# Optimization experiments

Hardware: AMD Instinct MI355X
Metric: run time of the kernel (lower is better)

Reference implementation:

```python
import jax, jax.numpy as jnp
import numpy as np

B, T, D = 4, 2048, 1024
EPS = 1e-5


def _layernorm(x, g, b):
    mu = jnp.mean(x, axis=-1, keepdims=True)
    var = jnp.var(x, axis=-1, keepdims=True)
    return (x - mu) * jax.lax.rsqrt(var + EPS) * g + b


def setup_inputs() -> dict:
    key = jax.random.key(0)
    ks = jax.random.split(key, 16)
    s = lambda fan_in: 1.0 / np.sqrt(fan_in)
    return {
        "x": jax.random.normal(ks[0], (B, T, D), dtype=jnp.float32),
        "ln1_g": jnp.ones((D,), jnp.float32),
        "ln1_b": jnp.zeros((D,), jnp.float32),
        "Wqkv": jax.random.uniform(ks[1], (D, 3 * D), jnp.float32, -s(D), s(D)),
        "bqkv": jnp.zeros((3 * D,), jnp.float32),
        "Wproj": jax.random.uniform(ks[2], (D, D), jnp.float32, -s(D), s(D)),
        "bproj": jnp.zeros((D,), jnp.float32),
        "ln2_g": jnp.ones((D,), jnp.float32),
        "ln2_b": jnp.zeros((D,), jnp.float32),
        "W1": jax.random.uniform(ks[3], (D, 4 * D), jnp.float32, -s(D), s(D)),
        "b1": jnp.zeros((4 * D,), jnp.float32),
        "W2": jax.random.uniform(ks[4], (4 * D, D), jnp.float32, -s(4 * D), s(4 * D)),
        "b2": jnp.zeros((D,), jnp.float32),
    }


def reference(x, ln1_g, ln1_b, Wqkv, bqkv, Wproj, bproj, ln2_g, ln2_b, W1, b1, W2, b2):
    # NOTE: no residual connections in the original Block.
    h = _layernorm(x, ln1_g, ln1_b)
    kqv = h @ Wqkv + bqkv                      # [B,T,3D]
    k, q, v = jnp.split(kqv, 3, axis=-1)       # split order: k, q, v
    # Original scales by 1/sqrt(k.size(-1)) AFTER transposing k -> 1/sqrt(T).
    scores = jnp.einsum("btd,bsd->bts", q, k) * (1.0 / np.sqrt(T))
    causal = jnp.tril(jnp.ones((T, T), dtype=bool))
    scores = jnp.where(causal, scores, -jnp.inf)
    attn = jax.nn.softmax(scores, axis=-1)
    a = jnp.einsum("bts,bsd->btd", attn, v)
    a = a @ Wproj + bproj
    h2 = _layernorm(a, ln2_g, ln2_b)
    m = jax.nn.gelu(h2 @ W1 + b1, approximate=True)
    return m @ W2 + b2
```

## Files before the change

kernel.cpp:

```cpp
#include <hip/hip_runtime.h>
#include <hip/hip_bf16.h>

typedef __hip_bfloat16 bf16;
typedef __bf16 bf16x8 __attribute__((ext_vector_type(8)));
typedef __bf16 bf16x4 __attribute__((ext_vector_type(4)));
typedef __bf16 bf16x2 __attribute__((ext_vector_type(2)));
typedef float f32x4 __attribute__((ext_vector_type(4)));

static constexpr int Bq = 4, Tq = 2048, Dq = 1024;

__device__ inline float b2f(bf16 h) { return __bfloat162float(h); }
__device__ inline bf16 f2b(float f) { return __float2bfloat16(f); }

__device__ __forceinline__ void gload_lds16(const bf16* g, bf16* lds_wave_base) {
    __builtin_amdgcn_global_load_lds((const __attribute__((address_space(1))) void*)g,
                                     (__attribute__((address_space(3))) void*)lds_wave_base,
                                     16, 0, 0);
}

__device__ __forceinline__ float fast_gelu(float x) {
    float u = x * (0.7978845608028654f + 0.03567740814183427f * x * x);
    float e = __builtin_amdgcn_exp2f(-2.885390081777927f * u);
    return x * __builtin_amdgcn_rcpf(1.f + e);
}

__device__ inline void ld4f(const float* p, float* v) {
    float4 t = *reinterpret_cast<const float4*>(p);
    v[0] = t.x; v[1] = t.y; v[2] = t.z; v[3] = t.w;
}
__device__ inline void ld4f(const bf16* p, float* v) {
    bf16x4 t = *reinterpret_cast<const bf16x4*>(p);
    v[0] = (float)t[0]; v[1] = (float)t[1]; v[2] = (float)t[2]; v[3] = (float)t[3];
}

template <typename Tin>
__device__ __forceinline__ void ln_body(const Tin* __restrict__ x, const float* __restrict__ g,
                                        const float* __restrict__ b, bf16* __restrict__ out,
                                        int row, float* sred)
{
    const int tid = threadIdx.x;
    const int s0 = tid * 4;
    const Tin* xr = x + (size_t)row * Dq;
    bf16* orow = out + (size_t)row * Dq;
    float v[4], gv[4], bv[4];
    ld4f(xr + s0, v);
    ld4f(g + s0, gv);
    ld4f(b + s0, bv);
    float sum = v[0] + v[1] + v[2] + v[3];
    float sq = v[0]*v[0] + v[1]*v[1] + v[2]*v[2] + v[3]*v[3];
    for (int o = 32; o > 0; o >>= 1) { sum += __shfl_xor(sum, o); sq += __shfl_xor(sq, o); }
    const int w = tid >> 6;
    if ((tid & 63) == 0) { sred[w] = sum; sred[4 + w] = sq; }
    __syncthreads();
    const float ts = sred[0] + sred[1] + sred[2] + sred[3];
    const float tq = sred[4] + sred[5] + sred[6] + sred[7];
    const float mean = ts / Dq;
    const float rs = rsqrtf(tq / Dq - mean * mean + 1e-5f);
    bf16x4 o4;
    #pragma unroll
    for (int i = 0; i < 4; ++i) o4[i] = (__bf16)((v[i] - mean) * rs * gv[i] + bv[i]);
    *reinterpret_cast<bf16x4*>(orow + s0) = o4;
}

__global__ void ln_kernel(const bf16* __restrict__ x, const float* __restrict__ g,
                          const float* __restrict__ b, bf16* __restrict__ out)
{
    __shared__ float sred[8];
    ln_body(x, g, b, out, blockIdx.x, sred);
}

__global__ void prep_kernel(const float* __restrict__ x, const float* __restrict__ g,
                            const float* __restrict__ b, bf16* __restrict__ h,
                            const float* __restrict__ Wqkv, bf16* __restrict__ WqkvT,
                            const float* __restrict__ Wproj, bf16* __restrict__ WprojT,
                            const float* __restrict__ W1, bf16* __restrict__ W1T,
                            const float* __restrict__ W2, bf16* __restrict__ W2T)
{
    __shared__ float smem[64 * 65];
    int id = blockIdx.x;
    if (id < 8192) { ln_body(x, g, b, h, id, smem); return; }
    id -= 8192;
    const float* src; bf16* dst; long ldin, ldout; int gx;
    if (id < 768)       { src = Wqkv;  dst = WqkvT;  ldin = 3072; ldout = 1024; gx = 48; }
    else if (id < 1024) { id -= 768;  src = Wproj; dst = WprojT; ldin = 1024; ldout = 1024; gx = 16; }
    else if (id < 2048) { id -= 1024; src = W1;    dst = W1T;    ldin = 4096; ldout = 1024; gx = 64; }
    else                { id -= 2048; src = W2;    dst = W2T;    ldin = 1024; ldout = 4096; gx = 16; }
    const int c0 = (id % gx) * 64, r0 = (id / gx) * 64;
    const int tid = threadIdx.x;
    const int tx = tid & 63, ty = tid >> 6;
    float (*tile)[65] = reinterpret_cast<float(*)[65]>(smem);
    #pragma unroll
    for (int i = 0; i < 16; ++i) {
        int r = ty + i * 4;
        tile[r][tx] = src[(size_t)(r0 + r) * ldin + c0 + tx];
    }
    __syncthreads();
    const int px = tid & 31, cy = tid >> 5;
    #pragma unroll
    for (int i = 0; i < 8; ++i) {
        int cc = cy + i * 8;
        bf16x2 p;
        p[0] = (__bf16)tile[px * 2][cc];
        p[1] = (__bf16)tile[px * 2 + 1][cc];
        *reinterpret_cast<bf16x2*>(&dst[(size_t)(c0 + cc) * ldout + r0 + px * 2]) = p;
    }
}

template <int ACT, int TRI, int CK, int FR>
__global__ void gemm128(const bf16* __restrict__ A, const bf16* __restrict__ Bt,
                        const float* __restrict__ bias,
                        bf16* __restrict__ Cb, float* __restrict__ Cf,
                        int K, long lda, long ldb, long ldc,
                        long sA, long sB, long sC, float scale,
                        const bf16* __restrict__ vsrc, bf16* __restrict__ vdst)
{
    __shared__ bf16 As[128 * 64];
    __shared__ bf16 Bs[128 * 64];

    int bx, by;
    if (TRI) {
        const int lin = blockIdx.x;
        if (lin >= 136) {
            const int idx = lin - 136;
            const int c0 = (idx & 15) * 64, r0 = (idx >> 4) * 64;
            const bf16* ip = vsrc + (size_t)blockIdx.z * ((size_t)Tq * 3072);
            bf16* op = vdst + (size_t)blockIdx.z * ((size_t)Dq * Tq);
            bf16 (*tile)[66] = reinterpret_cast<bf16(*)[66]>(As);
            const int tid = threadIdx.x;
            const int tx = tid & 31, ty = tid >> 5;
            #pragma unroll
            for (int i = 0; i < 8; ++i) {
                int r = ty + i * 8;
                *reinterpret_cast<bf16x2*>(&tile[r][tx * 2]) =
                    *reinterpret_cast<const bf16x2*>(&ip[(size_t)(r0 + r) * 3072 + c0 + tx * 2]);
            }
            __syncthreads();
            #pragma unroll
            for (int i = 0; i < 8; ++i) {
                int cc = ty + i * 8;
                bf16x2 p;
                p[0] = tile[tx * 2][cc];
                p[1] = tile[tx * 2 + 1][cc];
                *reinterpret_cast<bf16x2*>(&op[(size_t)(c0 + cc) * 2048 + r0 + tx * 2]) = p;
            }
            return;
        }
        int t = (int)((sqrtf(8.f * lin + 1.f) - 1.f) * 0.5f);
        while ((t + 1) * (t + 2) / 2 <= lin) ++t;
        while (t * (t + 1) / 2 > lin) --t;
        by = t; bx = lin - t * (t + 1) / 2;
    } else {
        const int gx = gridDim.x, gy = gridDim.y;
        const int lin = blockIdx.x + gx * blockIdx.y;
        const int band = lin & 7;
        const int idx = lin >> 3;
        bx = idx % gx;
        by = band * (gy >> 3) + idx / gx;
    }

    const int m0 = by * 128, n0 = bx * 128;
    const int Kend = CK ? min(K, m0 + 128) : K;

    const bf16* Ab = A + (size_t)blockIdx.z * sA;
    const bf16* Bb = Bt + (size_t)blockIdx.z * sB;
    const int tid = threadIdx.x;
    const int wid = tid >> 6, lane = tid & 63;
    const int wr = wid >> 1, wc = wid & 1;
    const int l15 = lane & 15, quad = lane >> 4;

    const int rloc = lane >> 3, slot = lane & 7;
    const bf16* agp = Ab + (size_t)(m0 + wid * 32 + rloc) * lda + (slot ^ rloc) * 8;
    const bf16* bgp = Bb + (size_t)(n0 + wid * 32 + rloc) * ldb + (slot ^ rloc) * 8;
    bf16* awb = As + wid * 32 * 64;
    bf16* bwb = Bs + wid * 32 * 64;

    const int afo = (wr * 64 + l15) * 64 + ((quad ^ (l15 & 7)) * 8);
    const int bfo = (wc * 64 + l15) * 64 + ((quad ^ (l15 & 7)) * 8);

    f32x4 acc[4][4];
    #pragma unroll
    for (int i = 0; i < 4; ++i)
        #pragma unroll
        for (int j = 0; j < 4; ++j) acc[i][j] = (f32x4){0.f, 0.f, 0.f, 0.f};

    f32x4 acc_l[4];
    bf16x8 ones;
    if (FR) {
        #pragma unroll
        for (int i = 0; i < 4; ++i) acc_l[i] = (f32x4){0.f, 0.f, 0.f, 0.f};
        #pragma unroll
        for (int i = 0; i < 8; ++i) ones[i] = (__bf16)1.0f;
    }

    for (int k0 = 0; k0 < Kend; k0 += 64) {
        #pragma unroll
        for (int i = 0; i < 4; ++i) {
            gload_lds16(agp + k0 + (size_t)(i * 8) * lda, awb + i * 8 * 64);
            gload_lds16(bgp + k0 + (size_t)(i * 8) * ldb, bwb + i * 8 * 64);
        }
        __syncthreads();

        bf16x8 af0[4], bf0[4], af1[4], bf1[4];
        #pragma unroll
        for (int i = 0; i < 4; ++i) {
            af0[i] = *reinterpret_cast<const bf16x8*>(As + (afo ^ 0)  + i * 1024);
            af1[i] = *reinterpret_cast<const bf16x8*>(As + (afo ^ 32) + i * 1024);
        }
        #pragma unroll
        for (int j = 0; j < 4; ++j) {
            bf0[j] = *reinterpret_cast<const bf16x8*>(Bs + (bfo ^ 0)  + j * 1024);
            bf1[j] = *reinterpret_cast<const bf16x8*>(Bs + (bfo ^ 32) + j * 1024);
        }
        #pragma unroll
        for (int i = 0; i < 4; ++i)
            #pragma unroll
            for (int j = 0; j < 4; ++j)
                acc[i][j] = __builtin_amdgcn_mfma_f32_16x16x32_bf16(af0[i], bf0[j], acc[i][j], 0, 0, 0);
        if (FR) {
            #pragma unroll
            for (int i = 0; i < 4; ++i)
                acc_l[i] = __builtin_amdgcn_mfma_f32_16x16x32_bf16(af0[i], ones, acc_l[i], 0, 0, 0);
        }
        #pragma unroll
        for (int i = 0; i < 4; ++i)
            #pragma unroll
            for (int j = 0; j < 4; ++j)
                acc[i][j] = __builtin_amdgcn_mfma_f32_16x16x32_bf16(af1[i], bf1[j], acc[i][j], 0, 0, 0);
        if (FR) {
            #pragma unroll
            for (int i = 0; i < 4; ++i)
                acc_l[i] = __builtin_amdgcn_mfma_f32_16x16x32_bf16(af1[i], ones, acc_l[i], 0, 0, 0);
        }

        __syncthreads();
    }

    #pragma unroll
    for (int i = 0; i < 4; ++i) {
        const int row = m0 + wr * 64 + i * 16 + quad * 4;
        #pragma unroll
        for (int j = 0; j < 4; ++j) {
            const int col = n0 + wc * 64 + j * 16 + l15;
            const float bv = bias ? bias[col] : 0.f;
            #pragma unroll
            for (int r = 0; r < 4; ++r) {
                float vv = scale * acc[i][j][r] + bv;
                if (ACT == 1) vv = fast_gelu(vv);
                else if (ACT == 2)
                    vv = (col <= row + r) ? __builtin_amdgcn_exp2f(1.4426950408889634f * vv) : 0.f;
                if (FR) vv *= __builtin_amdgcn_rcpf(acc_l[i][r]);
                const size_t idx2 = (size_t)(row + r) * ldc + col + (size_t)blockIdx.z * sC;
                if (Cf) Cf[idx2] = vv;
                else    Cb[idx2] = f2b(vv);
            }
        }
    }
}

template <int ACT>
__global__ __launch_bounds__(512, 2) void gemm256(
        const bf16* __restrict__ A, const bf16* __restrict__ Bt,
        const float* __restrict__ bias, bf16* __restrict__ C,
        int K, long lda, long ldb, long ldc)
{
    __shared__ bf16 As[2][256 * 64];
    __shared__ bf16 Bs[2][256 * 64];

    const int gx = gridDim.x, gy = gridDim.y;
    const int lin = blockIdx.x + gx * blockIdx.y;
    const int band = lin & 7;
    const int idx = lin >> 3;
    const int bx = idx % gx;
    const int by = band * (gy >> 3) + idx / gx;
    const int m0 = by * 256, n0 = bx * 256;

    const int tid = threadIdx.x;
    const int wid = tid >> 6, lane = tid & 63;
    const int wr = wid >> 2, wc = wid & 3;
    const int l15 = lane & 15, quad = lane >> 4;
    const int rloc = lane >> 3, slot = lane & 7;

    const bf16* agp = A + (size_t)(m0 + wid * 8 + rloc) * lda + (slot ^ rloc) * 8;
    const bf16* bgp = Bt + (size_t)(n0 + wid * 8 + rloc) * ldb + (slot ^ rloc) * 8;

    auto issueA = [&](int buf, int t2, int R) {
        gload_lds16(agp + (size_t)R * lda + t2 * 64, &As[buf][(R + wid * 8) * 64]);
    };
    auto issueB = [&](int buf, int t2, int R) {
        gload_lds16(bgp + (size_t)R * ldb + t2 * 64, &Bs[buf][(R + wid * 8) * 64]);
    };

    const int xg = (quad ^ (l15 & 7)) * 8;
    const int afo = (wr * 128 + l15) * 64 + xg;
    const int bfo = (wc * 64 + l15) * 64 + xg;

    f32x4 acc[8][4];
    #pragma unroll
    for (int i = 0; i < 8; ++i)
        #pragma unroll
        for (int j = 0; j < 4; ++j) acc[i][j] = (f32x4){0.f, 0.f, 0.f, 0.f};

    bf16x8 ax[4], ay[4], b0r[4], btr[4];

    const int nt = K >> 6;

#define RD_A(buf, rh, ks, dst)                                                            \
    { _Pragma("unroll")                                                                   \
      for (int i_ = 0; i_ < 4; ++i_)                                                      \
          dst[i_] = *reinterpret_cast<const bf16x8*>(                                     \
              &As[buf][(afo + (rh) * 4096 + i_ * 1024) ^ ((ks) * 32)]); }
#define RD_B(buf, ks, dst)                                                                \
    { _Pragma("unroll")                                                                   \
      for (int j_ = 0; j_ < 4; ++j_)                                                      \
          dst[j_] = *reinterpret_cast<const bf16x8*>(                                     \
              &Bs[buf][(bfo + j_ * 1024) ^ ((ks) * 32)]); }
#define MF(rh, Aset, Bset)                                                                \
    { __builtin_amdgcn_s_setprio(1);                                                      \
      _Pragma("unroll")                                                                   \
      for (int i_ = 0; i_ < 4; ++i_)                                                      \
          _Pragma("unroll")                                                               \
          for (int j_ = 0; j_ < 4; ++j_)                                                  \
              acc[(rh) * 4 + i_][j_] = __builtin_amdgcn_mfma_f32_16x16x32_bf16(           \
                  Aset[i_], Bset[j_], acc[(rh) * 4 + i_][j_], 0, 0, 0);                   \
      __builtin_amdgcn_s_setprio(0); }
#define BAR()    __builtin_amdgcn_s_barrier()
#define CFENCE() asm volatile("" ::: "memory")
#define LGKM(n)  asm volatile("s_waitcnt lgkmcnt(" #n ")" ::: "memory")

    issueA(0, 0, 0); issueA(0, 0, 128);
    issueB(0, 0, 0); issueB(0, 0, 64); issueB(0, 0, 128); issueB(0, 0, 192);
    issueA(0, 0, 64); issueA(0, 0, 192);
    asm volatile("s_waitcnt vmcnt(2)" ::: "memory");
    BAR(); CFENCE();
    RD_A(0, 0, 0, ax);
    RD_B(0, 0, b0r);

#define TILE_BODY(bufp, bufq, tn, PRE)                                                    \
                           \
    if (PRE) { issueA(bufq, tn, 0); issueA(bufq, tn, 128);                                \
               issueB(bufq, tn, 0); issueB(bufq, tn, 64); }                               \
    RD_A(bufp, 0, 1, ay); RD_B(bufp, 1, btr);                                             \
    BAR();                                                                                \
    LGKM(8);                                                                              \
    MF(0, ax, b0r);                                                                       \
    if (PRE) asm volatile("s_waitcnt vmcnt(4)" ::: "memory");                             \
    else     asm volatile("s_waitcnt vmcnt(0)" ::: "memory");                             \
    BAR(); CFENCE();                                                                      \
                         \
    if (PRE) { issueB(bufq, tn, 128); issueB(bufq, tn, 192); }                            \
    RD_A(bufp, 1, 0, ax);                                                                 \
    BAR();                                                                                \
    LGKM(4);                                                                              \
    MF(0, ay, btr);                                                                       \
    BAR();                                                                                \
                           \
    if (PRE) { issueA(bufq, tn, 64); issueA(bufq, tn, 192); }                             \
    RD_A(bufp, 1, 1, ay); RD_B(bufp, 1, btr);                                             \
    BAR();                                                                                \
    LGKM(8);                                                                              \
    MF(1, ax, b0r);                                                                       \
    BAR();                                                                                \
               \
    LGKM(0);                                                                              \
    MF(1, ay, btr);                                                                       \
    if (PRE) asm volatile("s_waitcnt vmcnt(2)" ::: "memory");                             \
    else     asm volatile("s_waitcnt vmcnt(0)" ::: "memory");                             \
    BAR(); CFENCE();                                                                      \
    if (PRE) { RD_A(bufq, 0, 0, ax); RD_B(bufq, 0, b0r); }

    for (int t = 0; t < nt; t += 2) {
        TILE_BODY(0, 1, t + 1, true);
        const bool pre2 = (t + 2) < nt;
        TILE_BODY(1, 0, t + 2, pre2);
    }
#undef TILE_BODY
#undef RD_A
#undef RD_B
#undef MF
#undef BAR
#undef CFENCE
#undef LGKM

    #pragma unroll
    for (int i = 0; i < 8; ++i) {
        const int row = m0 + wr * 128 + i * 16 + quad * 4;
        #pragma unroll
        for (int j = 0; j < 4; ++j) {
            const int col = n0 + wc * 64 + j * 16 + l15;
            const float bv = bias ? bias[col] : 0.f;
            #pragma unroll
            for (int r = 0; r < 4; ++r) {
                float vv = acc[i][j][r] + bv;
                if (ACT == 1) vv = fast_gelu(vv);
                C[(size_t)(row + r) * ldc + col] = f2b(vv);
            }
        }
    }
}

extern "C" void kernel_launch(void* const* d_in, const int* in_sizes, int n_in,
                              void* d_out, int out_size, void* d_ws, size_t ws_size,
                              hipStream_t stream)
{
    (void)in_sizes; (void)n_in; (void)out_size; (void)ws_size;
    const float* x     = (const float*)d_in[0];
    const float* ln1g  = (const float*)d_in[1];
    const float* ln1b  = (const float*)d_in[2];
    const float* Wqkv  = (const float*)d_in[3];
    const float* bqkv  = (const float*)d_in[4];
    const float* Wproj = (const float*)d_in[5];
    const float* bproj = (const float*)d_in[6];
    const float* ln2g  = (const float*)d_in[7];
    const float* ln2b  = (const float*)d_in[8];
    const float* W1    = (const float*)d_in[9];
    const float* b1    = (const float*)d_in[10];
    const float* W2    = (const float*)d_in[11];
    const float* b2    = (const float*)d_in[12];
    float* out = (float*)d_out;

    char* ws = (char*)d_ws;
    size_t off = 0;
    auto alloc = [&](size_t elems) { bf16* p = (bf16*)(ws + off); off += elems * sizeof(bf16); return p; };
    bf16* WqkvT  = alloc(3072UL * 1024);
    bf16* WprojT = alloc(1024UL * 1024);
    bf16* W1T    = alloc(4096UL * 1024);
    bf16* W2T    = alloc(1024UL * 4096);
    bf16* h      = alloc(8192UL * 1024);
    bf16* kqv    = alloc(8192UL * 3072);
    bf16* vT     = alloc(4UL * 1024 * 2048);
    bf16* attn   = alloc(4UL * 2048 * 2048);
    bf16* a   = h;
    bf16* p   = kqv;
    bf16* h2  = kqv + 8192UL * 1024;
    bf16* m   = kqv + 2UL * 8192 * 1024;

    const long T3D = (long)Tq * 3072, TT = (long)Tq * Tq, DT = (long)Dq * Tq, TD = (long)Tq * Dq;

    prep_kernel<<<11264, 256, 0, stream>>>(x, ln1g, ln1b, h,
                                           Wqkv, WqkvT, Wproj, WprojT, W1, W1T, W2, W2T);

    gemm256<0><<<dim3(12, 32, 1), 512, 0, stream>>>(h, WqkvT, bqkv, kqv,
        1024, 1024L, 1024L, 3072L);

    gemm128<2,1,0,0><<<dim3(648, 1, 4), 256, 0, stream>>>(kqv + 1024, kqv, nullptr, attn, nullptr,
        1024, 3072L, 3072L, 2048L, T3D, T3D, TT, 0.022097086912079608f, kqv + 2048, vT);

    gemm128<0,0,1,1><<<dim3(8, 16, 4), 256, 0, stream>>>(attn, vT, nullptr, a, nullptr,
        2048, 2048L, 2048L, 1024L, TT, DT, TD, 1.f, nullptr, nullptr);

    gemm128<0,0,0,0><<<dim3(8, 64, 1), 256, 0, stream>>>(a, WprojT, bproj, p, nullptr,
        1024, 1024L, 1024L, 1024L, 0L, 0L, 0L, 1.f, nullptr, nullptr);

    ln_kernel<<<8192, 256, 0, stream>>>(p, ln2g, ln2b, h2);

    gemm256<1><<<dim3(16, 32, 1), 512, 0, stream>>>(h2, W1T, b1, m,
        1024, 1024L, 1024L, 4096L);

    gemm128<0,0,0,0><<<dim3(8, 64, 1), 256, 0, stream>>>(m, W2T, b2, nullptr, out,
        4096, 4096L, 4096L, 1024L, 0L, 0L, 0L, 1.f, nullptr, nullptr);
}
```

Measured before the change: 545.7 us.

## Simplify gemm256 pipeline to one barrier per tile and drop occupancy hint

Replaces the hand-interleaved four-phase schedule, with its staggered partial global-to-LDS loads, lgkmcnt waits and multiple barriers per K-tile, with a simpler schedule. Each tile now issues all eight next-tile loads at once mid-compute, interleaves LDS fragment reads with half-sized MFMA groups, and syncs once at the end with vmcnt(0). It also removes the 2-blocks-per-CU launch-bounds hint, which lets the compiler use more registers. The intent is to cut barrier overhead. The cost is less fine-grained latency hiding, and possibly lower occupancy if register use rises.

```diff
diff --git a/kernel.cpp b/kernel.cpp
--- a/kernel.cpp
+++ b/kernel.cpp
@@ -258,7 +258,7 @@
 }
 
 template <int ACT>
-__global__ __launch_bounds__(512, 2) void gemm256(
+__global__ __launch_bounds__(512) void gemm256(
         const bf16* __restrict__ A, const bf16* __restrict__ Bt,
         const float* __restrict__ bias, bf16* __restrict__ C,
         int K, long lda, long ldb, long ldc)
@@ -300,7 +300,7 @@
         #pragma unroll
         for (int j = 0; j < 4; ++j) acc[i][j] = (f32x4){0.f, 0.f, 0.f, 0.f};
 
-    bf16x8 ax[4], ay[4], b0r[4], btr[4];
+    bf16x8 aA[4], aB[4], B0[4], B1[4];
 
     const int nt = K >> 6;
 
@@ -314,59 +314,42 @@
       for (int j_ = 0; j_ < 4; ++j_)                                                      \
           dst[j_] = *reinterpret_cast<const bf16x8*>(                                     \
               &Bs[buf][(bfo + j_ * 1024) ^ ((ks) * 32)]); }
-#define MF(rh, Aset, Bset)                                                                \
+#define MF8(rh, Aset, Bset, I0)                                                           \
     { __builtin_amdgcn_s_setprio(1);                                                      \
       _Pragma("unroll")                                                                   \
-      for (int i_ = 0; i_ < 4; ++i_)                                                      \
+      for (int i_ = (I0); i_ < (I0) + 2; ++i_)                                            \
           _Pragma("unroll")                                                               \
           for (int j_ = 0; j_ < 4; ++j_)                                                  \
               acc[(rh) * 4 + i_][j_] = __builtin_amdgcn_mfma_f32_16x16x32_bf16(           \
                   Aset[i_], Bset[j_], acc[(rh) * 4 + i_][j_], 0, 0, 0);                   \
       __builtin_amdgcn_s_setprio(0); }
+#define STAGE8(buf, t2)                                                                   \
+    { issueA(buf, t2, 0); issueA(buf, t2, 64); issueA(buf, t2, 128); issueA(buf, t2, 192);\
+      issueB(buf, t2, 0); issueB(buf, t2, 64); issueB(buf, t2, 128); issueB(buf, t2, 192); }
 #define BAR()    __builtin_amdgcn_s_barrier()
 #define CFENCE() asm volatile("" ::: "memory")
-#define LGKM(n)  asm volatile("s_waitcnt lgkmcnt(" #n ")" ::: "memory")
-
-    issueA(0, 0, 0); issueA(0, 0, 128);
-    issueB(0, 0, 0); issueB(0, 0, 64); issueB(0, 0, 128); issueB(0, 0, 192);
-    issueA(0, 0, 64); issueA(0, 0, 192);
-    asm volatile("s_waitcnt vmcnt(2)" ::: "memory");
-    BAR(); CFENCE();
-    RD_A(0, 0, 0, ax);
-    RD_B(0, 0, b0r);
-
-#define TILE_BODY(bufp, bufq, tn, PRE)                                                    \
-                           \
-    if (PRE) { issueA(bufq, tn, 0); issueA(bufq, tn, 128);                                \
-               issueB(bufq, tn, 0); issueB(bufq, tn, 64); }                               \
-    RD_A(bufp, 0, 1, ay); RD_B(bufp, 1, btr);                                             \
-    BAR();                                                                                \
-    LGKM(8);                                                                              \
-    MF(0, ax, b0r);                                                                       \
-    if (PRE) asm volatile("s_waitcnt vmcnt(4)" ::: "memory");                             \
-    else     asm volatile("s_waitcnt vmcnt(0)" ::: "memory");                             \
-    BAR(); CFENCE();                                                                      \
-                         \
-    if (PRE) { issueB(bufq, tn, 128); issueB(bufq, tn, 192); }                            \
-    RD_A(bufp, 1, 0, ax);                                                                 \
-    BAR();                                                                                \
-    LGKM(4);                                                                              \
-    MF(0, ay, btr);                                                                       \
-    BAR();                                                                                \
-                           \
-    if (PRE) { issueA(bufq, tn, 64); issueA(bufq, tn, 192); }                             \
-    RD_A(bufp, 1, 1, ay); RD_B(bufp, 1, btr);                                             \
-    BAR();                                                                                \
-    LGKM(8);                                                                              \
-    MF(1, ax, b0r);                                                                       \
-    BAR();                                                                                \
-               \
-    LGKM(0);                                                                              \
-    MF(1, ay, btr);                                                                       \
-    if (PRE) asm volatile("s_waitcnt vmcnt(2)" ::: "memory");                             \
-    else     asm volatile("s_waitcnt vmcnt(0)" ::: "memory");                             \
-    BAR(); CFENCE();                                                                      \
-    if (PRE) { RD_A(bufq, 0, 0, ax); RD_B(bufq, 0, b0r); }
+#define VMCNT0() asm volatile("s_waitcnt vmcnt(0)" ::: "memory")
+
+    STAGE8(0, 0);
+    VMCNT0();
+    CFENCE(); BAR(); CFENCE();
+
+#define TILE_BODY(bp, bq, tn, PRE)                                                        \
+    RD_A(bp, 0, 0, aA); RD_B(bp, 0, B0); RD_B(bp, 1, B1);                                 \
+    MF8(0, aA, B0, 0);                                                                    \
+    RD_A(bp, 0, 1, aB);                                                                   \
+    MF8(0, aA, B0, 2);                                                                    \
+    MF8(0, aB, B1, 0);                                                                    \
+    RD_A(bp, 1, 0, aA);                                                                   \
+    if (PRE) STAGE8(bq, tn);                                                              \
+    MF8(0, aB, B1, 2);                                                                    \
+    MF8(1, aA, B0, 0);                                                                    \
+    RD_A(bp, 1, 1, aB);                                                                   \
+    MF8(1, aA, B0, 2);                                                                    \
+    MF8(1, aB, B1, 0);                                                                    \
+    MF8(1, aB, B1, 2);                                                                    \
+    VMCNT0();                                                                             \
+    CFENCE(); BAR(); CFENCE();
 
     for (int t = 0; t < nt; t += 2) {
         TILE_BODY(0, 1, t + 1, true);
@@ -376,10 +359,11 @@
 #undef TILE_BODY
 #undef RD_A
 #undef RD_B
-#undef MF
+#undef MF8
+#undef STAGE8
 #undef BAR
 #undef CFENCE
-#undef LGKM
+#undef VMCNT0
 
     #pragma unroll
     for (int i = 0; i < 8; ++i) {
```

Result: faster. 484.5 us (-11.2%).
